# Kernel optimization log

Hardware: AMD Instinct MI355X
Metric: run time of the kernel (lower is better)

Reference implementation:

```python
import jax, jax.numpy as jnp
import numpy as np

N = 100000       # nodes
E = 1600000      # edges (avg degree 16)
IN_DIM = 64
HID_DIM = 128
OUT_DIM = 64

def setup_inputs() -> dict:
    key = jax.random.key(0)
    k = jax.random.split(key, 8)
    inp = jax.random.normal(k[0], (IN_DIM, N), dtype=jnp.float32)
    src = jax.random.randint(k[1], (E,), 0, N, dtype=jnp.int32)
    dst = jax.random.randint(k[2], (E,), 0, N, dtype=jnp.int32)
    # Linear params (torch nn.Linear: y = x @ W.T + b)
    s1 = 1.0 / np.sqrt(IN_DIM)
    W1 = jax.random.uniform(k[3], (HID_DIM, IN_DIM), jnp.float32, -s1, s1)
    b1 = jax.random.uniform(k[4], (HID_DIM,), jnp.float32, -s1, s1)
    s2 = 1.0 / np.sqrt(HID_DIM)
    W2 = jax.random.uniform(k[5], (OUT_DIM, HID_DIM), jnp.float32, -s2, s2)
    b2 = jax.random.uniform(k[6], (OUT_DIM,), jnp.float32, -s2, s2)
    return {"inp": inp, "src": src, "dst": dst, "W1": W1, "b1": b1, "W2": W2, "b2": b2}

def reference(inp, src, dst, W1, b1, W2, b2):
    # inp: [in_dim, N] (module passes transposed features)
    X = inp.T                                   # [N, in_dim] node features
    # update_all(copy_src, sum): gather src features, scatter-add at dst
    agg = jax.ops.segment_sum(X[src], dst, num_segments=X.shape[0])  # [N, in_dim]
    h = jax.nn.relu(agg @ W1.T + b1)            # [N, hidden]
    out = h @ W2.T + b2                         # [N, out_dim]
    return out.T                                 # [out_dim, N] (final .t())
```

## Files before the change

kernel.cpp:

```cpp
#include <hip/hip_runtime.h>
#include <hip/hip_bf16.h>
#include <stdint.h>

typedef unsigned short ushort_t;
using short8   = __attribute__((ext_vector_type(8))) short;
using float4v  = __attribute__((ext_vector_type(4))) float;

#define BSH    6
#define BUCKW  64
#define CAP    1536
#define NBMAX  2048

__device__ __forceinline__ float bf2f(ushort_t u) {
    union { unsigned int i; float f; } v;
    v.i = ((unsigned int)u) << 16;
    return v.f;
}
__device__ __forceinline__ ushort_t f2b(float f) {
    union { float f; unsigned int i; } v;
    v.f = f;
    unsigned int u = v.i;
    unsigned int r = (u + 0x7fffu + ((u >> 16) & 1u)) >> 16;
    return (ushort_t)r;
}

__global__ void transpose_k(const float* __restrict__ inp,
                            ushort_t* __restrict__ X, int N,
                            const float* __restrict__ W1,
                            const float* __restrict__ W2,
                            ushort_t* __restrict__ w1b,
                            ushort_t* __restrict__ w2b,
                            int* __restrict__ gcur, int NB) {
    if (blockIdx.x == 0) {
        for (int i = threadIdx.x; i < 8192; i += 256) {
            w1b[i] = f2b(W1[i]);
            w2b[i] = f2b(W2[i]);
        }
        for (int b = threadIdx.x; b < NB; b += 256) gcur[b] = b * CAP;
    }
    __shared__ float tile[64][65];
    int tx = threadIdx.x & 63;
    int ty = threadIdx.x >> 6;
    int n0 = blockIdx.x * 64;
#pragma unroll
    for (int r = 0; r < 16; ++r) {
        int d = ty * 16 + r;
        int n = n0 + tx;
        if (n < N) tile[d][tx] = inp[(size_t)d * N + n];
    }
    __syncthreads();
#pragma unroll
    for (int r = 0; r < 16; ++r) {
        int nl = ty * 16 + r;
        int n  = n0 + nl;
        if (n < N) X[(size_t)n * 64 + tx] = f2b(tile[tx][nl]);
    }
}

__global__ __launch_bounds__(1024) void bin_k(
        const int* __restrict__ src, const int* __restrict__ dst,
        int* __restrict__ gcur, unsigned* __restrict__ bin, int E, int NB) {
    __shared__ int lcnt[NBMAX];
    __shared__ int gbase[NBMAX];
    __shared__ int lcur[NBMAX];
    int tid   = threadIdx.x;
    int chunk = (E + gridDim.x - 1) / gridDim.x;
    int s0 = blockIdx.x * chunk;
    int s1 = s0 + chunk;
    if (s1 > E) s1 = E;

    for (int b = tid; b < NB; b += 1024) lcnt[b] = 0;
    __syncthreads();

    for (int e = s0 + tid; e < s1; e += 1024)
        atomicAdd(&lcnt[dst[e] >> BSH], 1);
    __syncthreads();

    for (int b = tid; b < NB; b += 1024) {
        int c = lcnt[b];
        gbase[b] = c ? atomicAdd(&gcur[b], c) : 0;
        lcur[b]  = 0;
    }
    __syncthreads();

    for (int e = s0 + tid; e < s1; e += 1024) {
        int d = dst[e];
        int b = d >> BSH;
        int pos = gbase[b] + atomicAdd(&lcur[b], 1);
        if (pos < (b + 1) * CAP)
            bin[pos] = ((unsigned)(d & (BUCKW - 1)) << 24) | (unsigned)src[e];
    }
}

__global__ __launch_bounds__(256) void bagg_k(
        const ushort_t* __restrict__ X, const unsigned* __restrict__ bin,
        const int* __restrict__ gcur, float* __restrict__ agg, int N) {
    __shared__ unsigned sl[CAP];
    __shared__ int ecnt[BUCKW];
    __shared__ int sc[BUCKW];
    __shared__ int ecur[BUCKW];
    int tid = threadIdx.x;
    int b   = blockIdx.x;
    int lo  = b << BSH;

    int cnt = gcur[b] - b * CAP;
    if (cnt > CAP) cnt = CAP;
    const unsigned* bb = bin + (size_t)b * CAP;

    if (tid < BUCKW) ecnt[tid] = 0;
    __syncthreads();

    for (int i = tid; i < cnt; i += 256)
        atomicAdd(&ecnt[bb[i] >> 24], 1);
    __syncthreads();

    if (tid < BUCKW) sc[tid] = ecnt[tid];
    __syncthreads();
#pragma unroll
    for (int off = 1; off < BUCKW; off <<= 1) {
        int v = 0;
        if (tid < BUCKW && tid >= off) v = sc[tid - off];
        __syncthreads();
        if (tid < BUCKW) sc[tid] += v;
        __syncthreads();
    }
    if (tid < BUCKW) { sc[tid] -= ecnt[tid]; ecur[tid] = 0; }
    __syncthreads();

    for (int i = tid; i < cnt; i += 256) {
        unsigned p = bb[i];
        int nl  = (int)(p >> 24);
        int pos = sc[nl] + atomicAdd(&ecur[nl], 1);
        sl[pos] = p;
    }
    __syncthreads();

    int wave = tid >> 6;
    int lane = tid & 63;
    for (int n = wave; n < BUCKW; n += 4) {
        int node = lo + n;
        if (node >= N) break;
        int s0 = sc[n];
        int c  = ecnt[n];
        float a0 = 0.f, a1 = 0.f, a2 = 0.f, a3 = 0.f;
        int i = 0;
        for (; i + 7 < c; i += 8) {
            unsigned p0 = sl[s0 + i],     p1 = sl[s0 + i + 1];
            unsigned p2 = sl[s0 + i + 2], p3 = sl[s0 + i + 3];
            unsigned p4 = sl[s0 + i + 4], p5 = sl[s0 + i + 5];
            unsigned p6 = sl[s0 + i + 6], p7 = sl[s0 + i + 7];
            a0 += bf2f(X[(size_t)(p0 & 0xFFFFFFu) * 64 + lane]);
            a1 += bf2f(X[(size_t)(p1 & 0xFFFFFFu) * 64 + lane]);
            a2 += bf2f(X[(size_t)(p2 & 0xFFFFFFu) * 64 + lane]);
            a3 += bf2f(X[(size_t)(p3 & 0xFFFFFFu) * 64 + lane]);
            a0 += bf2f(X[(size_t)(p4 & 0xFFFFFFu) * 64 + lane]);
            a1 += bf2f(X[(size_t)(p5 & 0xFFFFFFu) * 64 + lane]);
            a2 += bf2f(X[(size_t)(p6 & 0xFFFFFFu) * 64 + lane]);
            a3 += bf2f(X[(size_t)(p7 & 0xFFFFFFu) * 64 + lane]);
        }
        for (; i < c; ++i)
            a0 += bf2f(X[(size_t)(sl[s0 + i] & 0xFFFFFFu) * 64 + lane]);
        agg[(size_t)node * 64 + lane] = (a0 + a1) + (a2 + a3);
    }
}

#define HPITCH 136

__global__ __launch_bounds__(256) void mlp_k(
        const float* __restrict__ agg,
        const ushort_t* __restrict__ W1, const float* __restrict__ b1,
        const ushort_t* __restrict__ W2, const float* __restrict__ b2,
        float* __restrict__ out, int N) {
    __shared__ ushort_t h_s[4][16 * HPITCH];

    int wave = threadIdx.x >> 6;
    int lane = threadIdx.x & 63;
    int row  = lane & 15;
    int quad = lane >> 4;
    int n0   = blockIdx.x * 64 + wave * 16;

    int anode = n0 + row;
    if (anode > N - 1) anode = N - 1;
    const float* ap = agg + (size_t)anode * 64 + quad * 8;

    short8 a0, a1;
    {
        float4v f0 = *(const float4v*)(ap);
        float4v f1 = *(const float4v*)(ap + 4);
        float4v f2 = *(const float4v*)(ap + 32);
        float4v f3 = *(const float4v*)(ap + 36);
#pragma unroll
        for (int j = 0; j < 4; ++j) {
            a0[j]     = (short)f2b(f0[j]);
            a0[j + 4] = (short)f2b(f1[j]);
            a1[j]     = (short)f2b(f2[j]);
            a1[j + 4] = (short)f2b(f3[j]);
        }
    }

    float4v zero = {0.f, 0.f, 0.f, 0.f};
    float4v acc[8];
#pragma unroll
    for (int nt = 0; nt < 8; ++nt) acc[nt] = zero;

#pragma unroll
    for (int nt = 0; nt < 8; ++nt) {
        const ushort_t* wp = W1 + (size_t)(nt * 16 + row) * 64 + quad * 8;
        short8 bf0 = *(const short8*)(wp);
        short8 bf1 = *(const short8*)(wp + 32);
        acc[nt] = __builtin_amdgcn_mfma_f32_16x16x32_bf16(a0, bf0, acc[nt], 0, 0, 0);
        acc[nt] = __builtin_amdgcn_mfma_f32_16x16x32_bf16(a1, bf1, acc[nt], 0, 0, 0);
    }

    ushort_t* hw = h_s[wave];
#pragma unroll
    for (int nt = 0; nt < 8; ++nt) {
        float bias = b1[nt * 16 + row];
#pragma unroll
        for (int r = 0; r < 4; ++r) {
            float v = acc[nt][r] + bias;
            v = v > 0.f ? v : 0.f;
            hw[(quad * 4 + r) * HPITCH + nt * 16 + row] = f2b(v);
        }
    }
    __syncthreads();

    short8 a2[4];
#pragma unroll
    for (int kt = 0; kt < 4; ++kt)
        a2[kt] = *(const short8*)(hw + row * HPITCH + kt * 32 + quad * 8);

    float4v acc2[4];
#pragma unroll
    for (int nt = 0; nt < 4; ++nt) acc2[nt] = zero;

#pragma unroll
    for (int nt = 0; nt < 4; ++nt) {
#pragma unroll
        for (int kt = 0; kt < 4; ++kt) {
            short8 bfr = *(const short8*)(W2 + (size_t)(nt * 16 + row) * 128 +
                                          kt * 32 + quad * 8);
            acc2[nt] = __builtin_amdgcn_mfma_f32_16x16x32_bf16(a2[kt], bfr, acc2[nt], 0, 0, 0);
        }
    }

    int node = n0 + quad * 4;
    if (node < N) {
#pragma unroll
        for (int nt = 0; nt < 4; ++nt) {
            int ko = nt * 16 + row;
            float bias = b2[ko];
            float4v pk;
#pragma unroll
            for (int r = 0; r < 4; ++r) pk[r] = acc2[nt][r] + bias;
            *(float4v*)(out + (size_t)ko * N + node) = pk;
        }
    }
}

extern "C" void kernel_launch(void* const* d_in, const int* in_sizes, int n_in,
                              void* d_out, int out_size, void* d_ws, size_t ws_size,
                              hipStream_t stream) {
    const float* inp = (const float*)d_in[0];
    const int*   src = (const int*)d_in[1];
    const int*   dst = (const int*)d_in[2];
    const float* W1  = (const float*)d_in[3];
    const float* b1  = (const float*)d_in[4];
    const float* W2  = (const float*)d_in[5];
    const float* b2  = (const float*)d_in[6];
    float* out = (float*)d_out;

    int N = in_sizes[0] / 64;
    int E = in_sizes[1];
    int NB = (N + BUCKW - 1) >> BSH;

    float*    agg  = (float*)d_ws;
    ushort_t* w1b  = (ushort_t*)((char*)d_ws + (size_t)N * 64 * sizeof(float));
    ushort_t* w2b  = w1b + 8192;
    int*      gcur = (int*)(w2b + 8192);

    char*     ob  = (char*)d_out;
    ushort_t* X   = (ushort_t*)ob;
    unsigned* bin = (unsigned*)(ob + (size_t)N * 64 * 2);

    int tb = (N + 63) / 64;
    transpose_k<<<tb, 256, 0, stream>>>(inp, X, N, W1, W2, w1b, w2b, gcur, NB);

    bin_k<<<128, 1024, 0, stream>>>(src, dst, gcur, bin, E, NB);
    bagg_k<<<NB, 256, 0, stream>>>(X, bin, gcur, agg, N);

    mlp_k<<<tb, 256, 0, stream>>>(agg, w1b, b1, w2b, b2, out, N);
}
```

Before: 212.5 us.

## Fuse transpose with binning and gather bf16 pairs with bf16 aggregate output

```diff
diff --git a/kernel.cpp b/kernel.cpp
--- a/kernel.cpp
+++ b/kernel.cpp
@@ -10,6 +10,8 @@
 #define BUCKW  64
 #define CAP    1536
 #define NBMAX  2048
+#define TPITCH 266
+#define BINB   128
 
 __device__ __forceinline__ float bf2f(ushort_t u) {
     union { unsigned int i; float f; } v;
@@ -23,78 +25,86 @@
     unsigned int r = (u + 0x7fffu + ((u >> 16) & 1u)) >> 16;
     return (ushort_t)r;
 }
-
-__global__ void transpose_k(const float* __restrict__ inp,
-                            ushort_t* __restrict__ X, int N,
-                            const float* __restrict__ W1,
-                            const float* __restrict__ W2,
-                            ushort_t* __restrict__ w1b,
-                            ushort_t* __restrict__ w2b,
-                            int* __restrict__ gcur, int NB) {
-    if (blockIdx.x == 0) {
-        for (int i = threadIdx.x; i < 8192; i += 256) {
-            w1b[i] = f2b(W1[i]);
-            w2b[i] = f2b(W2[i]);
-        }
-        for (int b = threadIdx.x; b < NB; b += 256) gcur[b] = b * CAP;
-    }
-    __shared__ float tile[64][65];
-    int tx = threadIdx.x & 63;
-    int ty = threadIdx.x >> 6;
-    int n0 = blockIdx.x * 64;
-#pragma unroll
-    for (int r = 0; r < 16; ++r) {
-        int d = ty * 16 + r;
-        int n = n0 + tx;
-        if (n < N) tile[d][tx] = inp[(size_t)d * N + n];
-    }
-    __syncthreads();
-#pragma unroll
-    for (int r = 0; r < 16; ++r) {
-        int nl = ty * 16 + r;
-        int n  = n0 + nl;
-        if (n < N) X[(size_t)n * 64 + tx] = f2b(tile[tx][nl]);
-    }
-}
-
-__global__ __launch_bounds__(1024) void bin_k(
+__device__ __forceinline__ float blo2f(unsigned v) {
+    union { unsigned i; float f; } u; u.i = v << 16; return u.f;
+}
+__device__ __forceinline__ float bhi2f(unsigned v) {
+    union { unsigned i; float f; } u; u.i = v & 0xFFFF0000u; return u.f;
+}
+
+__global__ __launch_bounds__(1024) void prep_k(
+        const float* __restrict__ inp, ushort_t* __restrict__ X, int N,
+        const float* __restrict__ W1, const float* __restrict__ W2,
+        ushort_t* __restrict__ w1b, ushort_t* __restrict__ w2b,
         const int* __restrict__ src, const int* __restrict__ dst,
-        int* __restrict__ gcur, unsigned* __restrict__ bin, int E, int NB) {
-    __shared__ int lcnt[NBMAX];
-    __shared__ int gbase[NBMAX];
-    __shared__ int lcur[NBMAX];
-    int tid   = threadIdx.x;
-    int chunk = (E + gridDim.x - 1) / gridDim.x;
-    int s0 = blockIdx.x * chunk;
-    int s1 = s0 + chunk;
-    if (s1 > E) s1 = E;
-
-    for (int b = tid; b < NB; b += 1024) lcnt[b] = 0;
-    __syncthreads();
-
-    for (int e = s0 + tid; e < s1; e += 1024)
-        atomicAdd(&lcnt[dst[e] >> BSH], 1);
-    __syncthreads();
-
-    for (int b = tid; b < NB; b += 1024) {
-        int c = lcnt[b];
-        gbase[b] = c ? atomicAdd(&gcur[b], c) : 0;
-        lcur[b]  = 0;
-    }
-    __syncthreads();
-
-    for (int e = s0 + tid; e < s1; e += 1024) {
-        int d = dst[e];
-        int b = d >> BSH;
-        int pos = gbase[b] + atomicAdd(&lcur[b], 1);
-        if (pos < (b + 1) * CAP)
-            bin[pos] = ((unsigned)(d & (BUCKW - 1)) << 24) | (unsigned)src[e];
+        int* __restrict__ gcur, unsigned* __restrict__ bin, int E,
+        int NB, int TB) {
+    __shared__ __align__(16) char smem[64 * TPITCH * 2];
+    int tid = threadIdx.x;
+
+    if ((int)blockIdx.x < TB) {
+        if (blockIdx.x == 0) {
+            for (int i = tid; i < 8192; i += 1024) {
+                w1b[i] = f2b(W1[i]);
+                w2b[i] = f2b(W2[i]);
+            }
+        }
+        ushort_t* tile = (ushort_t*)smem;
+        int w    = tid >> 6;
+        int lane = tid & 63;
+        int n0   = blockIdx.x * 256;
+        int col  = (w >> 2) * 64 + lane;
+        int nc   = n0 + col;
+#pragma unroll
+        for (int r = 0; r < 16; ++r) {
+            int d = (w & 3) * 16 + r;
+            if (nc < N) tile[d * TPITCH + col] = f2b(inp[(size_t)d * N + nc]);
+        }
+        __syncthreads();
+#pragma unroll
+        for (int r = 0; r < 16; ++r) {
+            int nl = w * 16 + r;
+            int n  = n0 + nl;
+            if (n < N) X[(size_t)n * 64 + lane] = tile[lane * TPITCH + nl];
+        }
+    } else {
+        int* lcnt  = (int*)smem;
+        int* gbase = lcnt + NBMAX;
+        int* lcur  = gbase + NBMAX;
+        int bid   = blockIdx.x - TB;
+        int chunk = (E + BINB - 1) / BINB;
+        int s0 = bid * chunk;
+        int s1 = s0 + chunk;
+        if (s1 > E) s1 = E;
+
+        for (int b = tid; b < NB; b += 1024) lcnt[b] = 0;
+        __syncthreads();
+
+        for (int e = s0 + tid; e < s1; e += 1024)
+            atomicAdd(&lcnt[dst[e] >> BSH], 1);
+        __syncthreads();
+
+        for (int b = tid; b < NB; b += 1024) {
+            int c = lcnt[b];
+            gbase[b] = c ? atomicAdd(&gcur[b], c) : 0;
+            lcur[b]  = 0;
+        }
+        __syncthreads();
+
+        for (int e = s0 + tid; e < s1; e += 1024) {
+            int d = dst[e];
+            int b = d >> BSH;
+            int pos = gbase[b] + atomicAdd(&lcur[b], 1);
+            if (pos < CAP)
+                bin[(size_t)b * CAP + pos] =
+                    ((unsigned)(d & (BUCKW - 1)) << 24) | (unsigned)src[e];
+        }
     }
 }
 
 __global__ __launch_bounds__(256) void bagg_k(
-        const ushort_t* __restrict__ X, const unsigned* __restrict__ bin,
-        const int* __restrict__ gcur, float* __restrict__ agg, int N) {
+        const unsigned* __restrict__ Xu, const unsigned* __restrict__ bin,
+        const int* __restrict__ gcur, unsigned* __restrict__ aggu, int N) {
     __shared__ unsigned sl[CAP];
     __shared__ int ecnt[BUCKW];
     __shared__ int sc[BUCKW];
@@ -103,7 +113,7 @@
     int b   = blockIdx.x;
     int lo  = b << BSH;
 
-    int cnt = gcur[b] - b * CAP;
+    int cnt = gcur[b];
     if (cnt > CAP) cnt = CAP;
     const unsigned* bb = bin + (size_t)b * CAP;
 
@@ -137,37 +147,64 @@
 
     int wave = tid >> 6;
     int lane = tid & 63;
+    int half = lane >> 5;
+    int c2   = lane & 31;
+
     for (int n = wave; n < BUCKW; n += 4) {
         int node = lo + n;
         if (node >= N) break;
         int s0 = sc[n];
         int c  = ecnt[n];
-        float a0 = 0.f, a1 = 0.f, a2 = 0.f, a3 = 0.f;
+        float alo0 = 0.f, ahi0 = 0.f, alo1 = 0.f, ahi1 = 0.f;
         int i = 0;
-        for (; i + 7 < c; i += 8) {
-            unsigned p0 = sl[s0 + i],     p1 = sl[s0 + i + 1];
-            unsigned p2 = sl[s0 + i + 2], p3 = sl[s0 + i + 3];
-            unsigned p4 = sl[s0 + i + 4], p5 = sl[s0 + i + 5];
-            unsigned p6 = sl[s0 + i + 6], p7 = sl[s0 + i + 7];
-            a0 += bf2f(X[(size_t)(p0 & 0xFFFFFFu) * 64 + lane]);
-            a1 += bf2f(X[(size_t)(p1 & 0xFFFFFFu) * 64 + lane]);
-            a2 += bf2f(X[(size_t)(p2 & 0xFFFFFFu) * 64 + lane]);
-            a3 += bf2f(X[(size_t)(p3 & 0xFFFFFFu) * 64 + lane]);
-            a0 += bf2f(X[(size_t)(p4 & 0xFFFFFFu) * 64 + lane]);
-            a1 += bf2f(X[(size_t)(p5 & 0xFFFFFFu) * 64 + lane]);
-            a2 += bf2f(X[(size_t)(p6 & 0xFFFFFFu) * 64 + lane]);
-            a3 += bf2f(X[(size_t)(p7 & 0xFFFFFFu) * 64 + lane]);
-        }
-        for (; i < c; ++i)
-            a0 += bf2f(X[(size_t)(sl[s0 + i] & 0xFFFFFFu) * 64 + lane]);
-        agg[(size_t)node * 64 + lane] = (a0 + a1) + (a2 + a3);
+        for (; i + 16 <= c; i += 16) {
+            unsigned p0 = sl[s0 + i +  0 + half], p1 = sl[s0 + i +  2 + half];
+            unsigned p2 = sl[s0 + i +  4 + half], p3 = sl[s0 + i +  6 + half];
+            unsigned p4 = sl[s0 + i +  8 + half], p5 = sl[s0 + i + 10 + half];
+            unsigned p6 = sl[s0 + i + 12 + half], p7 = sl[s0 + i + 14 + half];
+            unsigned v0 = Xu[(size_t)(p0 & 0xFFFFFFu) * 32 + c2];
+            unsigned v1 = Xu[(size_t)(p1 & 0xFFFFFFu) * 32 + c2];
+            unsigned v2 = Xu[(size_t)(p2 & 0xFFFFFFu) * 32 + c2];
+            unsigned v3 = Xu[(size_t)(p3 & 0xFFFFFFu) * 32 + c2];
+            unsigned v4 = Xu[(size_t)(p4 & 0xFFFFFFu) * 32 + c2];
+            unsigned v5 = Xu[(size_t)(p5 & 0xFFFFFFu) * 32 + c2];
+            unsigned v6 = Xu[(size_t)(p6 & 0xFFFFFFu) * 32 + c2];
+            unsigned v7 = Xu[(size_t)(p7 & 0xFFFFFFu) * 32 + c2];
+            alo0 += blo2f(v0); ahi0 += bhi2f(v0);
+            alo1 += blo2f(v1); ahi1 += bhi2f(v1);
+            alo0 += blo2f(v2); ahi0 += bhi2f(v2);
+            alo1 += blo2f(v3); ahi1 += bhi2f(v3);
+            alo0 += blo2f(v4); ahi0 += bhi2f(v4);
+            alo1 += blo2f(v5); ahi1 += bhi2f(v5);
+            alo0 += blo2f(v6); ahi0 += bhi2f(v6);
+            alo1 += blo2f(v7); ahi1 += bhi2f(v7);
+        }
+        for (; i + 2 <= c; i += 2) {
+            unsigned p = sl[s0 + i + half];
+            unsigned v = Xu[(size_t)(p & 0xFFFFFFu) * 32 + c2];
+            alo0 += blo2f(v); ahi0 += bhi2f(v);
+        }
+        if (i + half < c) {
+            unsigned p = sl[s0 + i + half];
+            unsigned v = Xu[(size_t)(p & 0xFFFFFFu) * 32 + c2];
+            alo1 += blo2f(v); ahi1 += bhi2f(v);
+        }
+        float alo = alo0 + alo1;
+        float ahi = ahi0 + ahi1;
+        float blo = __shfl(alo, lane + 32);
+        float bhi = __shfl(ahi, lane + 32);
+        if (half == 0) {
+            alo += blo; ahi += bhi;
+            aggu[(size_t)node * 32 + c2] =
+                (unsigned)f2b(alo) | ((unsigned)f2b(ahi) << 16);
+        }
     }
 }
 
 #define HPITCH 136
 
 __global__ __launch_bounds__(256) void mlp_k(
-        const float* __restrict__ agg,
+        const ushort_t* __restrict__ aggb,
         const ushort_t* __restrict__ W1, const float* __restrict__ b1,
         const ushort_t* __restrict__ W2, const float* __restrict__ b2,
         float* __restrict__ out, int N) {
@@ -181,22 +218,9 @@
 
     int anode = n0 + row;
     if (anode > N - 1) anode = N - 1;
-    const float* ap = agg + (size_t)anode * 64 + quad * 8;
-
-    short8 a0, a1;
-    {
-        float4v f0 = *(const float4v*)(ap);
-        float4v f1 = *(const float4v*)(ap + 4);
-        float4v f2 = *(const float4v*)(ap + 32);
-        float4v f3 = *(const float4v*)(ap + 36);
-#pragma unroll
-        for (int j = 0; j < 4; ++j) {
-            a0[j]     = (short)f2b(f0[j]);
-            a0[j + 4] = (short)f2b(f1[j]);
-            a1[j]     = (short)f2b(f2[j]);
-            a1[j + 4] = (short)f2b(f3[j]);
-        }
-    }
+    const ushort_t* ap = aggb + (size_t)anode * 64;
+    short8 a0 = *(const short8*)(ap + quad * 8);
+    short8 a1 = *(const short8*)(ap + 32 + quad * 8);
 
     float4v zero = {0.f, 0.f, 0.f, 0.f};
     float4v acc[8];
@@ -270,12 +294,12 @@
     const float* b2  = (const float*)d_in[6];
     float* out = (float*)d_out;
 
-    int N = in_sizes[0] / 64;
-    int E = in_sizes[1];
+    int N  = in_sizes[0] / 64;
+    int E  = in_sizes[1];
     int NB = (N + BUCKW - 1) >> BSH;
 
-    float*    agg  = (float*)d_ws;
-    ushort_t* w1b  = (ushort_t*)((char*)d_ws + (size_t)N * 64 * sizeof(float));
+    ushort_t* aggb = (ushort_t*)d_ws;
+    ushort_t* w1b  = aggb + (size_t)N * 64;
     ushort_t* w2b  = w1b + 8192;
     int*      gcur = (int*)(w2b + 8192);
 
@@ -283,11 +307,15 @@
     ushort_t* X   = (ushort_t*)ob;
     unsigned* bin = (unsigned*)(ob + (size_t)N * 64 * 2);
 
+    hipMemsetAsync(gcur, 0, NB * sizeof(int), stream);
+
+    int TB = (N + 255) / 256;
+    prep_k<<<TB + BINB, 1024, 0, stream>>>(inp, X, N, W1, W2, w1b, w2b,
+                                           src, dst, gcur, bin, E, NB, TB);
+
+    bagg_k<<<NB, 256, 0, stream>>>((const unsigned*)X, bin, gcur,
+                                   (unsigned*)aggb, N);
+
     int tb = (N + 63) / 64;
-    transpose_k<<<tb, 256, 0, stream>>>(inp, X, N, W1, W2, w1b, w2b, gcur, NB);
-
-    bin_k<<<128, 1024, 0, stream>>>(src, dst, gcur, bin, E, NB);
-    bagg_k<<<NB, 256, 0, stream>>>(X, bin, gcur, agg, N);
-
-    mlp_k<<<tb, 256, 0, stream>>>(agg, w1b, b1, w2b, b2, out, N);
-}
+    mlp_k<<<tb, 256, 0, stream>>>(aggb, w1b, b1, w2b, b2, out, N);
+}
```

Result: faster. 204.1 us (-4.0%).
